# Kernel optimization log

Hardware: AMD Instinct MI355X
Metric: run time of the kernel (lower is better)

## Reference

```python
import jax, jax.numpy as jnp
import numpy as np
import math

D, H, DK, DFF, B, T, K = 512, 8, 64, 2048, 8, 512, 31
P = 2 * T - 1  # rel-pos length


def _ln(x, g, b, eps=1e-5):
    mu = jnp.mean(x, -1, keepdims=True)
    var = jnp.var(x, -1, keepdims=True)
    return (x - mu) * jax.lax.rsqrt(var + eps) * g + b


def _silu(x):
    return x * jax.nn.sigmoid(x)


def _rel_shift(x):
    # x: [B,H,T,P] -> NeMo-style relative shift
    b, h, t, p = x.shape
    x = jnp.pad(x, ((0, 0), (0, 0), (0, 0), (1, 0)))
    x = x.reshape(b, h, p + 1, t)
    return x[:, :, 1:, :].reshape(b, h, t, p)


def _forward(x, pos_emb, ln1_g, ln1_b, ff1_w1, ff1_b1, ff1_w2, ff1_b2,
             lna_g, lna_b, wq, bq, wk, bk, wv, bv, wo, bo, wpos, pbu, pbv,
             lnc_g, lnc_b, pw1_w, pw1_b, dw_w, dw_b, cln_g, cln_b, pw2_w, pw2_b,
             ln2_g, ln2_b, ff2_w1, ff2_b1, ff2_w2, ff2_b2, lno_g, lno_b):
    b, t, d = x.shape
    h, dk = pbu.shape
    # FF1 (half-step residual)
    r = x
    y = _ln(x, ln1_g, ln1_b)
    y = _silu(y @ ff1_w1 + ff1_b1) @ ff1_w2 + ff1_b2
    r = r + 0.5 * y
    # Rel-pos multi-head attention
    y = _ln(r, lna_g, lna_b)
    q = (y @ wq + bq).reshape(b, t, h, dk)
    k = (y @ wk + bk).reshape(b, t, h, dk)
    v = (y @ wv + bv).reshape(b, t, h, dk)
    p = (pos_emb @ wpos).reshape(pos_emb.shape[0], -1, h, dk)[0]  # [P,H,dk]
    ac = jnp.einsum('bthd,bshd->bhts', q + pbu, k)
    bd = jnp.einsum('bthd,phd->bhtp', q + pbv, p)
    bd = _rel_shift(bd)[..., :t]
    attn = jax.nn.softmax((ac + bd) / math.sqrt(dk), axis=-1)
    o = jnp.einsum('bhts,bshd->bthd', attn, v).reshape(b, t, d) @ wo + bo
    r = r + o
    # Conformer convolution module (layer_norm variant)
    y = _ln(r, lnc_g, lnc_b)
    y = y @ pw1_w + pw1_b                       # [B,T,2D] pointwise conv1
    a, g = jnp.split(y, 2, axis=-1)
    y = a * jax.nn.sigmoid(g)                   # GLU over channels
    y = jnp.transpose(y, (0, 2, 1))             # [B,D,T]
    pad = (dw_w.shape[1] - 1) // 2
    y = jax.lax.conv_general_dilated(
        y, dw_w[:, None, :], (1,), [(pad, pad)],
        feature_group_count=d, dimension_numbers=('NCH', 'OIH', 'NCH'))
    y = y + dw_b[None, :, None]
    y = jnp.transpose(y, (0, 2, 1))             # [B,T,D]
    y = _ln(y, cln_g, cln_b)
    y = _silu(y) @ pw2_w + pw2_b                # pointwise conv2
    r = r + y
    # FF2 (half-step residual)
    y = _ln(r, ln2_g, ln2_b)
    y = _silu(y @ ff2_w1 + ff2_b1) @ ff2_w2 + ff2_b2
    r = r + 0.5 * y
    return _ln(r, lno_g, lno_b)


def setup_inputs() -> dict:
    key = jax.random.key(0)
    ks = iter(jax.random.split(key, 64))
    rn = lambda shape, s=0.05: jax.random.normal(next(ks), shape, dtype=jnp.float32) * s
    ones = lambda n: jnp.ones((n,), jnp.float32)
    zeros = lambda n: jnp.zeros((n,), jnp.float32)
    return dict(
        x=jax.random.normal(next(ks), (B, T, D), jnp.float32),
        pos_emb=jax.random.normal(next(ks), (1, P, D), jnp.float32),
        ln1_g=ones(D), ln1_b=zeros(D),
        ff1_w1=rn((D, DFF)), ff1_b1=zeros(DFF), ff1_w2=rn((DFF, D)), ff1_b2=zeros(D),
        lna_g=ones(D), lna_b=zeros(D),
        wq=rn((D, D)), bq=zeros(D), wk=rn((D, D)), bk=zeros(D),
        wv=rn((D, D)), bv=zeros(D), wo=rn((D, D)), bo=zeros(D),
        wpos=rn((D, D)), pbu=rn((H, DK)), pbv=rn((H, DK)),
        lnc_g=ones(D), lnc_b=zeros(D),
        pw1_w=rn((D, 2 * D)), pw1_b=zeros(2 * D),
        dw_w=rn((D, K)), dw_b=zeros(D),
        cln_g=ones(D), cln_b=zeros(D),
        pw2_w=rn((D, D)), pw2_b=zeros(D),
        ln2_g=ones(D), ln2_b=zeros(D),
        ff2_w1=rn((D, DFF)), ff2_b1=zeros(DFF), ff2_w2=rn((DFF, D)), ff2_b2=zeros(D),
        lno_g=ones(D), lno_b=zeros(D))


def reference(x, pos_emb, ln1_g, ln1_b, ff1_w1, ff1_b1, ff1_w2, ff1_b2,
              lna_g, lna_b, wq, bq, wk, bk, wv, bv, wo, bo, wpos, pbu, pbv,
              lnc_g, lnc_b, pw1_w, pw1_b, dw_w, dw_b, cln_g, cln_b, pw2_w, pw2_b,
              ln2_g, ln2_b, ff2_w1, ff2_b1, ff2_w2, ff2_b2, lno_g, lno_b):
    return _forward(x, pos_emb, ln1_g, ln1_b, ff1_w1, ff1_b1, ff1_w2, ff1_b2,
                    lna_g, lna_b, wq, bq, wk, bk, wv, bv, wo, bo, wpos, pbu, pbv,
                    lnc_g, lnc_b, pw1_w, pw1_b, dw_w, dw_b, cln_g, cln_b, pw2_w, pw2_b,
                    ln2_g, ln2_b, ff2_w1, ff2_b1, ff2_w2, ff2_b2, lno_g, lno_b)
```

## Files before the change

### kernel.cpp

```cpp
#include <hip/hip_runtime.h>
#include <hip/hip_bf16.h>

#define Bb 8
#define Tt 512
#define Dd 512
#define Hh 8
#define DKk 64
#define DFFf 2048
#define Pp 1023
#define KCc 31
#define BTt 4096
#define QS 1536

typedef __hip_bfloat16 bf16;
typedef __attribute__((ext_vector_type(8))) short short8;
typedef __attribute__((ext_vector_type(4))) short s4v;
typedef __attribute__((ext_vector_type(4))) float f32x4;

union BFU { __hip_bfloat16 h; short s; };
static __device__ __forceinline__ short bfbits(float f) {
    BFU u; u.h = __float2bfloat16(f); return u.s;
}
static __device__ __forceinline__ float bff(short s) {
    BFU u; u.s = s; return __bfloat162float(u.h);
}
static __device__ __forceinline__ unsigned pk2(float a, float b) {
    return (unsigned)(unsigned short)bfbits(a) | ((unsigned)(unsigned short)bfbits(b) << 16);
}

static __device__ __forceinline__ int dflag(const void* lg) {
    return ((const unsigned*)lg)[0] == 0x3F803F80u;
}

#define GLD16(g, l) __builtin_amdgcn_global_load_lds(                          \
    (const __attribute__((address_space(1))) void*)(g),                        \
    (__attribute__((address_space(3))) void*)(l), 16, 0, 0)

#define XCD_SWZ(bxs, bys)                                                     \
    int nwg_ = gridDim.x * gridDim.y;                                         \
    int w_ = blockIdx.y * gridDim.x + blockIdx.x;                             \
    int sw_ = (w_ & 7) * (nwg_ >> 3) + (w_ >> 3);                             \
    int bxs = sw_ % gridDim.x, bys = sw_ / gridDim.x;

struct CvtDesc { const void* src; unsigned n; unsigned off; unsigned startBlk; };
struct CvtArgs { CvtDesc d[32]; };

__global__ __launch_bounds__(256) void cvt_batch_k(CvtArgs args, int ncv,
                                                   bf16* __restrict__ dst,
                                                   const void* __restrict__ lg) {
    int bid = blockIdx.x;
    int ti = 0;
    while (ti + 1 < ncv && bid >= (int)args.d[ti + 1].startBlk) ti++;
    CvtDesc de = args.d[ti];
    unsigned i = (bid - de.startBlk) * 256u + threadIdx.x;
    if (i >= de.n) return;
    float v;
    if (dflag(lg)) v = __bfloat162float(((const bf16*)de.src)[i]);
    else           v = ((const float*)de.src)[i];
    dst[de.off + i] = __float2bfloat16(v);
}

struct TD { const void* src; unsigned doff, R, C, startBlk; };
struct TArgs { TD d[11]; };

__global__ __launch_bounds__(256) void transpose_batch_k(TArgs ta, bf16* __restrict__ wt,
                                                         const void* __restrict__ lg) {
    int bid = blockIdx.x;
    int ti = 0;
    while (ti + 1 < 11 && bid >= (int)ta.d[ti + 1].startBlk) ti++;
    TD t = ta.d[ti];
    int tile = bid - t.startBlk;
    int ntc = t.C >> 5;
    int tr = tile / ntc, tc = tile % ntc;
    __shared__ short tl[32][33];
    short* out = (short*)wt + t.doff;
    int tx = threadIdx.x & 31, ty = threadIdx.x >> 5;
    int fl = dflag(lg);
#pragma unroll
    for (int i = 0; i < 32; i += 8) {
        size_t idx = (size_t)(tr * 32 + ty + i) * t.C + tc * 32 + tx;
        short v;
        if (fl) v = ((const short*)t.src)[idx];
        else    v = bfbits(((const float*)t.src)[idx]);
        tl[ty + i][tx] = v;
    }
    __syncthreads();
#pragma unroll
    for (int i = 0; i < 32; i += 8)
        out[(size_t)(tc * 32 + ty + i) * t.R + tr * 32 + tx] = tl[tx][ty + i];
}

__global__ __launch_bounds__(256) void prep_misc_k(const void* __restrict__ dww, bf16* __restrict__ dwT,
                                                   const void* __restrict__ bq, const void* __restrict__ bk,
                                                   const void* __restrict__ bv, bf16* __restrict__ bqkv,
                                                   bf16* __restrict__ pF,
                                                   const void* __restrict__ lg) {
    int i = blockIdx.x * 256 + threadIdx.x;
    int fl = dflag(lg);
    if (i < Dd * KCc) {
        int d = i / KCc, j = i % KCc;
        short v = fl ? ((const short*)dww)[i] : bfbits(((const float*)dww)[i]);
        ((short*)dwT)[j * Dd + d] = v;
    } else if (i < Dd * KCc + QS) {
        int j = i - Dd * KCc;
        const void* s = (j < 512) ? bq : ((j < 1024) ? bk : bv);
        int idx = j & 511;
        short v = fl ? ((const short*)s)[idx] : bfbits(((const float*)s)[idx]);
        ((short*)bqkv)[j] = v;
    } else {
        int j2 = i - Dd * KCc - QS;
        if (j2 < 512) {
            int h = j2 >> 6, ksp = (j2 >> 5) & 1, qd = (j2 >> 3) & 3, e = j2 & 7;
            ((short*)pF)[(size_t)h * 65536 + ksp * 512 + qd * 128 + e] = 0;
        }
    }
}

template <int SILU>
__global__ __launch_bounds__(256) void ln_k(const float* __restrict__ in,
                                            const bf16* __restrict__ g,
                                            const bf16* __restrict__ b,
                                            bf16* __restrict__ out) {
    int row = blockIdx.x;
    int tid = threadIdx.x;
    float2 v = ((const float2*)(in + (size_t)row * Dd))[tid];
    float s = v.x + v.y;
    float ss = v.x * v.x + v.y * v.y;
#pragma unroll
    for (int off = 32; off > 0; off >>= 1) {
        s += __shfl_xor(s, off);
        ss += __shfl_xor(ss, off);
    }
    __shared__ float red[2][4];
    int wid = tid >> 6;
    if ((tid & 63) == 0) { red[0][wid] = s; red[1][wid] = ss; }
    __syncthreads();
    float S = red[0][0] + red[0][1] + red[0][2] + red[0][3];
    float SS = red[1][0] + red[1][1] + red[1][2] + red[1][3];
    float mean = S * (1.0f / Dd);
    float var = SS * (1.0f / Dd) - mean * mean;
    float rstd = rsqrtf(var + 1e-5f);
    unsigned gp = *(const unsigned*)((const short*)g + 2 * tid);
    unsigned bp = *(const unsigned*)((const short*)b + 2 * tid);
    float o0 = (v.x - mean) * rstd * bff((short)(gp & 0xFFFF)) + bff((short)(bp & 0xFFFF));
    float o1 = (v.y - mean) * rstd * bff((short)(gp >> 16)) + bff((short)(bp >> 16));
    if (SILU) {
        o0 = o0 / (1.0f + __expf(-o0));
        o1 = o1 / (1.0f + __expf(-o1));
    }
    *(unsigned*)((short*)out + (size_t)row * Dd + 2 * tid) = pk2(o0, o1);
}

__global__ __launch_bounds__(256) void ln_x_k(const void* __restrict__ x,
                                              const bf16* __restrict__ g,
                                              const bf16* __restrict__ b,
                                              float* __restrict__ r,
                                              bf16* __restrict__ out,
                                              const void* __restrict__ lg) {
    int row = blockIdx.x;
    int tid = threadIdx.x;
    size_t base = (size_t)row * Dd;
    float v0, v1;
    if (dflag(lg)) {
        unsigned xp = *(const unsigned*)((const short*)x + base + 2 * tid);
        v0 = bff((short)(xp & 0xFFFF));
        v1 = bff((short)(xp >> 16));
    } else {
        float2 xv = ((const float2*)((const float*)x + base))[tid];
        v0 = xv.x; v1 = xv.y;
    }
    ((float2*)(r + base))[tid] = make_float2(v0, v1);
    float s = v0 + v1;
    float ss = v0 * v0 + v1 * v1;
#pragma unroll
    for (int off = 32; off > 0; off >>= 1) {
        s += __shfl_xor(s, off);
        ss += __shfl_xor(ss, off);
    }
    __shared__ float red[2][4];
    int wid = tid >> 6;
    if ((tid & 63) == 0) { red[0][wid] = s; red[1][wid] = ss; }
    __syncthreads();
    float S = red[0][0] + red[0][1] + red[0][2] + red[0][3];
    float SS = red[1][0] + red[1][1] + red[1][2] + red[1][3];
    float mean = S * (1.0f / Dd);
    float var = SS * (1.0f / Dd) - mean * mean;
    float rstd = rsqrtf(var + 1e-5f);
    unsigned gp = *(const unsigned*)((const short*)g + 2 * tid);
    unsigned bp = *(const unsigned*)((const short*)b + 2 * tid);
    float o0 = (v0 - mean) * rstd * bff((short)(gp & 0xFFFF)) + bff((short)(bp & 0xFFFF));
    float o1 = (v1 - mean) * rstd * bff((short)(gp >> 16)) + bff((short)(bp >> 16));
    *(unsigned*)((short*)out + base + 2 * tid) = pk2(o0, o1);
}

__global__ __launch_bounds__(256) void ln_out_k(const float* __restrict__ in,
                                                const bf16* __restrict__ g,
                                                const bf16* __restrict__ b,
                                                void* __restrict__ out,
                                                const void* __restrict__ lg) {
    int row = blockIdx.x;
    int tid = threadIdx.x;
    size_t base = (size_t)row * Dd;
    float2 v = ((const float2*)(in + base))[tid];
    float s = v.x + v.y;
    float ss = v.x * v.x + v.y * v.y;
#pragma unroll
    for (int off = 32; off > 0; off >>= 1) {
        s += __shfl_xor(s, off);
        ss += __shfl_xor(ss, off);
    }
    __shared__ float red[2][4];
    int wid = tid >> 6;
    if ((tid & 63) == 0) { red[0][wid] = s; red[1][wid] = ss; }
    __syncthreads();
    float S = red[0][0] + red[0][1] + red[0][2] + red[0][3];
    float SS = red[1][0] + red[1][1] + red[1][2] + red[1][3];
    float mean = S * (1.0f / Dd);
    float var = SS * (1.0f / Dd) - mean * mean;
    float rstd = rsqrtf(var + 1e-5f);
    unsigned gp = *(const unsigned*)((const short*)g + 2 * tid);
    unsigned bp = *(const unsigned*)((const short*)b + 2 * tid);
    float o0 = (v.x - mean) * rstd * bff((short)(gp & 0xFFFF)) + bff((short)(bp & 0xFFFF));
    float o1 = (v.y - mean) * rstd * bff((short)(gp >> 16)) + bff((short)(bp >> 16));
    if (dflag(lg)) {
        *(unsigned*)((short*)out + base + 2 * tid) = pk2(o0, o1);
    } else {
        ((float2*)((float*)out + base))[tid] = make_float2(o0, o1);
    }
}

template <int BM, int BN, int BK, int WM, int WN, typename CT, int ACT, int RES, int VT>
__global__ __launch_bounds__(256) void gemm_mfma_k(const bf16* __restrict__ Abf,
                                                   const bf16* __restrict__ WT,
                                                   const bf16* __restrict__ bias,
                                                   const float* __restrict__ resid,
                                                   CT* __restrict__ C,
                                                   bf16* __restrict__ vt,
                                                   bf16* __restrict__ kf,
                                                   bf16* __restrict__ qf,
                                                   int M, int N, int Kd, float alpha) {
    constexpr int MT = WM / 16, NT = WN / 16;
    constexpr int WX = BN / WN;
    constexpr int CPB = BK / 8;
    constexpr int KS = BK / 32;
    __shared__ __align__(16) short As[BM * BK];
    __shared__ __align__(16) short Bs[BN * BK];
    int tid = threadIdx.x;
    int wid = tid >> 6, lane = tid & 63;
    int lm = lane & 15, quad = lane >> 4;
    int wy = wid / WX, wx = wid % WX;
    XCD_SWZ(bxs, bys);
    int bm = bys * BM, bn = bxs * BN;
    const short* Ag = (const short*)Abf;
    const short* Bg = (const short*)WT;

    f32x4 acc[MT][NT] = {};

    for (int k0 = 0; k0 < Kd; k0 += BK) {
#pragma unroll
        for (int it = 0; it < BM * CPB / 256; it++) {
            int c = it * 256 + tid;
            int row = c / CPB;
            int q = (c % CPB) ^ (row & 7);
            int gr = bm + row;
            if (gr > M - 1) gr = M - 1;
            GLD16(Ag + (size_t)gr * Kd + k0 + q * 8, As + (it * 256 + wid * 64) * 8);
        }
#pragma unroll
        for (int it = 0; it < BN * CPB / 256; it++) {
            int c = it * 256 + tid;
            int row = c / CPB;
            int q = (c % CPB) ^ (row & 7);
            GLD16(Bg + (size_t)(bn + row) * Kd + k0 + q * 8, Bs + (it * 256 + wid * 64) * 8);
        }
        __syncthreads();
        short8 af[MT][KS], bfv[NT][KS];
#pragma unroll
        for (int mt = 0; mt < MT; mt++) {
            int row = wy * WM + mt * 16 + lm;
#pragma unroll
            for (int ks = 0; ks < KS; ks++)
                af[mt][ks] = *(const short8*)&As[row * BK + (((ks * 4 + quad) ^ (row & 7)) * 8)];
        }
#pragma unroll
        for (int nt = 0; nt < NT; nt++) {
            int row = wx * WN + nt * 16 + lm;
#pragma unroll
            for (int ks = 0; ks < KS; ks++)
                bfv[nt][ks] = *(const short8*)&Bs[row * BK + (((ks * 4 + quad) ^ (row & 7)) * 8)];
        }
#pragma unroll
        for (int ks = 0; ks < KS; ks++)
#pragma unroll
            for (int mt = 0; mt < MT; mt++)
#pragma unroll
                for (int nt = 0; nt < NT; nt++)
                    acc[mt][nt] = __builtin_amdgcn_mfma_f32_16x16x32_bf16(af[mt][ks], bfv[nt][ks], acc[mt][nt], 0, 0, 0);
        __syncthreads();
    }

#pragma unroll
    for (int mt = 0; mt < MT; mt++) {
#pragma unroll
        for (int nt = 0; nt < NT; nt++) {
            int gcol = bn + wx * WN + nt * 16 + lm;
            int growb = bm + wy * WM + mt * 16 + quad * 4;
            if (VT == 1 && gcol >= 1024) {
                int hd = gcol - 1024;
                int h = hd >> 6, d = hd & 63;
                int b = growb >> 9, tt = growb & 511;
                float bi = __bfloat162float(bias[gcol]);
                s4v pk;
#pragma unroll
                for (int r = 0; r < 4; r++) pk[r] = bfbits(acc[mt][nt][r] + bi);
                size_t base = (((((size_t)b * 8 + h) * 16 + (tt >> 5)) * 4 + (d >> 4)) * 64 +
                               (((tt >> 3) & 3) * 16 + (d & 15))) * 8 + (tt & 7);
                *(s4v*)((short*)vt + base) = pk;
            } else if (VT == 1 && gcol >= 512) {
                int hd = gcol - 512;
                int h = hd >> 6, kk = hd & 63;
                int b = growb >> 9, tt = growb & 511;
                float bi = __bfloat162float(bias[gcol]);
                size_t base2 = ((((size_t)b * 8 + h) * 32 + (tt >> 4)) * 2 + (kk >> 5)) * 512;
                int qd = (kk >> 3) & 3, e = kk & 7;
#pragma unroll
                for (int r = 0; r < 4; r++)
                    ((short*)kf)[base2 + (size_t)(qd * 16 + (tt & 15) + r) * 8 + e] =
                        bfbits(acc[mt][nt][r] + bi);
            } else if (VT == 1) {
                int h = gcol >> 6, kk = gcol & 63;
                int b = growb >> 9, tt = growb & 511;
                float bi = __bfloat162float(bias[gcol]);
                size_t base2 = ((((size_t)b * 8 + h) * 32 + (tt >> 4)) * 2 + (kk >> 5)) * 512;
                int qd = (kk >> 3) & 3, e = kk & 7;
#pragma unroll
                for (int r = 0; r < 4; r++)
                    ((short*)qf)[base2 + (size_t)(qd * 16 + (tt & 15) + r) * 8 + e] =
                        bfbits(acc[mt][nt][r] + bi);
            } else if (VT == 2) {
                int h = gcol >> 6, kk = gcol & 63;
                int ksp = kk >> 5, qd = (kk >> 3) & 3, e = kk & 7;
#pragma unroll
                for (int r = 0; r < 4; r++) {
                    int grow = growb + r;
                    if (grow >= M) continue;
                    int p1 = grow + 1;
                    int J = p1 >> 4, lmz = p1 & 15;
                    ((short*)vt)[(size_t)(h * 64 + J) * 1024 + ksp * 512 + (qd * 16 + lmz) * 8 + e] =
                        bfbits(acc[mt][nt][r]);
                }
            } else {
#pragma unroll
                for (int r = 0; r < 4; r++) {
                    int grow = growb + r;
                    if (grow >= M) continue;
                    float v = acc[mt][nt][r];
                    if (bias) v += __bfloat162float(bias[gcol]);
                    if (ACT == 1) v = v / (1.0f + __expf(-v));
                    if (RES == 1) v = resid[(size_t)grow * N + gcol] + alpha * v;
                    C[(size_t)grow * N + gcol] = (CT)v;
                }
            }
        }
    }
}

__global__ __launch_bounds__(256) void gemm_glu_k(const bf16* __restrict__ Abf,
                                                  const bf16* __restrict__ WT,
                                                  const bf16* __restrict__ bias,
                                                  bf16* __restrict__ C) {
    constexpr int BM = 64, BN = 64, BK = 64, WM = 32, WN = 32;
    constexpr int MT = WM / 16, NT = WN / 16, WX = BN / WN, CPB = BK / 8, KS = BK / 32;
    __shared__ __align__(16) short As[BM * BK];
    __shared__ __align__(16) short Bs[2 * BN * BK];
    int tid = threadIdx.x;
    int wid = tid >> 6, lane = tid & 63;
    int lm = lane & 15, quad = lane >> 4;
    int wy = wid / WX, wx = wid % WX;
    XCD_SWZ(bxs, bys);
    int bm = bys * BM, bn = bxs * BN;
    const short* Ag = (const short*)Abf;
    const short* Bg = (const short*)WT;

    f32x4 acc[MT][NT][2] = {};

    for (int k0 = 0; k0 < Dd; k0 += BK) {
#pragma unroll
        for (int it = 0; it < BM * CPB / 256; it++) {
            int c = it * 256 + tid;
            int row = c / CPB;
            int q = (c % CPB) ^ (row & 7);
            GLD16(Ag + (size_t)(bm + row) * Dd + k0 + q * 8, As + (it * 256 + wid * 64) * 8);
        }
#pragma unroll
        for (int it = 0; it < 2 * BN * CPB / 256; it++) {
            int c = it * 256 + tid;
            int row = c / CPB;
            int q = (c % CPB) ^ (row & 7);
            int wrow = (row < BN) ? (bn + row) : (512 + bn + row - BN);
            GLD16(Bg + (size_t)wrow * Dd + k0 + q * 8, Bs + (it * 256 + wid * 64) * 8);
        }
        __syncthreads();
        short8 af[MT][KS], bfv[NT][2][KS];
#pragma unroll
        for (int mt = 0; mt < MT; mt++) {
            int row = wy * WM + mt * 16 + lm;
#pragma unroll
            for (int ks = 0; ks < KS; ks++)
                af[mt][ks] = *(const short8*)&As[row * BK + (((ks * 4 + quad) ^ (row & 7)) * 8)];
        }
#pragma unroll
        for (int nt = 0; nt < NT; nt++) {
#pragma unroll
            for (int hf = 0; hf < 2; hf++) {
                int row = hf * BN + wx * WN + nt * 16 + lm;
#pragma unroll
                for (int ks = 0; ks < KS; ks++)
                    bfv[nt][hf][ks] = *(const short8*)&Bs[row * BK + (((ks * 4 + quad) ^ (row & 7)) * 8)];
            }
        }
#pragma unroll
        for (int ks = 0; ks < KS; ks++)
#pragma unroll
            for (int mt = 0; mt < MT; mt++)
#pragma unroll
                for (int nt = 0; nt < NT; nt++) {
                    acc[mt][nt][0] = __builtin_amdgcn_mfma_f32_16x16x32_bf16(af[mt][ks], bfv[nt][0][ks], acc[mt][nt][0], 0, 0, 0);
                    acc[mt][nt][1] = __builtin_amdgcn_mfma_f32_16x16x32_bf16(af[mt][ks], bfv[nt][1][ks], acc[mt][nt][1], 0, 0, 0);
                }
        __syncthreads();
    }

#pragma unroll
    for (int mt = 0; mt < MT; mt++) {
#pragma unroll
        for (int nt = 0; nt < NT; nt++) {
#pragma unroll
            for (int r = 0; r < 4; r++) {
                int grow = bm + wy * WM + mt * 16 + quad * 4 + r;
                int gcol = bn + wx * WN + nt * 16 + lm;
                float va = acc[mt][nt][0][r] + __bfloat162float(bias[gcol]);
                float vg = acc[mt][nt][1][r] + __bfloat162float(bias[512 + gcol]);
                float v = va / (1.0f + __expf(-vg));
                C[(size_t)grow * Dd + gcol] = __float2bfloat16(v);
            }
        }
    }
}

#define PST 520
#define OST 72

__global__ __launch_bounds__(256, 4) void attn_mfma_k(const bf16* __restrict__ qF,
                                                      const bf16* __restrict__ kF,
                                                      const bf16* __restrict__ pF,
                                                      const bf16* __restrict__ vF,
                                                      const bf16* __restrict__ pbu,
                                                      const bf16* __restrict__ pbv,
                                                      bf16* __restrict__ out) {
    __shared__ __align__(16) short Pl[16 * PST];
    __shared__ __align__(16) float redm[16][4];
    __shared__ __align__(16) float reds[16][4];
    int tid = threadIdx.x;
    int wid = tid >> 6;
    int lane = tid & 63;
    int lm = lane & 15;
    int quad = lane >> 4;
    int bidx = (blockIdx.x & 7) * 256 + (blockIdx.x >> 3);
    int b = bidx >> 8;
    int h = (bidx >> 5) & 7;
    int t0 = (bidx & 31) * 16;

    short8 qu[2], qv[2];
    {
        const short* qa = (const short*)qF +
            ((size_t)((b * 8 + h) * 32 + (t0 >> 4)) * 2) * 512 + lane * 8;
        const short* pbus = (const short*)pbu + h * DKk + quad * 8;
        const short* pbvs = (const short*)pbv + h * DKk + quad * 8;
#pragma unroll
        for (int ksp = 0; ksp < 2; ksp++) {
            short8 raw = *(const short8*)(qa + ksp * 512);
            short8 bu = *(const short8*)(pbus + ksp * 32);
            short8 bv = *(const short8*)(pbvs + ksp * 32);
#pragma unroll
            for (int j = 0; j < 8; j++) {
                float qf2 = bff(raw[j]);
                qu[ksp][j] = bfbits(qf2 + bff(bu[j]));
                qv[ksp][j] = bfbits(qf2 + bff(bv[j]));
            }
        }
    }

    const float scale = 0.125f;
    const short* kFs = (const short*)kF + ((size_t)(b * 8 + h) * 32) * 1024;
    const short* pFs = (const short*)pF + ((size_t)h * 64) * 1024;
    int Jbase = 32 - (t0 >> 4) + wid * 8;

    f32x4 dprev = {0.f, 0.f, 0.f, 0.f};
    {
        const short* pa = pFs + (size_t)(Jbase - 1) * 1024 + lane * 8;
        dprev = __builtin_amdgcn_mfma_f32_16x16x32_bf16(qv[0], *(const short8*)pa, dprev, 0, 0, 0);
        dprev = __builtin_amdgcn_mfma_f32_16x16x32_bf16(qv[1], *(const short8*)(pa + 512), dprev, 0, 0, 0);
    }

    f32x4 sreg[8];
#pragma unroll
    for (int i = 0; i < 8; i++) {
        int st = wid * 8 + i;
        f32x4 ac = {0.f, 0.f, 0.f, 0.f};
        f32x4 dcur = {0.f, 0.f, 0.f, 0.f};
        const short* ka = kFs + (size_t)st * 1024 + lane * 8;
        const short* pa = pFs + (size_t)(Jbase + i) * 1024 + lane * 8;
        ac = __builtin_amdgcn_mfma_f32_16x16x32_bf16(qu[0], *(const short8*)ka, ac, 0, 0, 0);
        ac = __builtin_amdgcn_mfma_f32_16x16x32_bf16(qu[1], *(const short8*)(ka + 512), ac, 0, 0, 0);
        dcur = __builtin_amdgcn_mfma_f32_16x16x32_bf16(qv[0], *(const short8*)pa, dcur, 0, 0, 0);
        dcur = __builtin_amdgcn_mfma_f32_16x16x32_bf16(qv[1], *(const short8*)(pa + 512), dcur, 0, 0, 0);
#pragma unroll
        for (int r = 0; r < 4; r++) {
            int m = quad * 4 + r;
            int j = (lm - m) & 15;
            int srcl = quad * 16 + j;
            float b2 = __shfl(dcur[r], srcl, 64);
            float b1 = __shfl(dprev[r], srcl, 64);
            float bd = (lm >= m) ? b2 : b1;
            sreg[i][r] = scale * (ac[r] + bd);
        }
        dprev = dcur;
    }

    float mrow[4];
#pragma unroll
    for (int r = 0; r < 4; r++) {
        float m = sreg[0][r];
#pragma unroll
        for (int i = 1; i < 8; i++) m = fmaxf(m, sreg[i][r]);
#pragma unroll
        for (int off = 1; off < 16; off <<= 1) m = fmaxf(m, __shfl_xor(m, off));
        mrow[r] = m;
    }
    if (lm < 4) {
        float v = (lm == 0) ? mrow[0] : (lm == 1) ? mrow[1] : (lm == 2) ? mrow[2] : mrow[3];
        redm[quad * 4 + lm][wid] = v;
    }
    __syncthreads();

    float gm[4], srow[4];
#pragma unroll
    for (int r = 0; r < 4; r++) {
        float4 mv = *(const float4*)&redm[quad * 4 + r][0];
        gm[r] = fmaxf(fmaxf(mv.x, mv.y), fmaxf(mv.z, mv.w));
        srow[r] = 0.f;
    }
#pragma unroll
    for (int i = 0; i < 8; i++) {
        int col = (wid * 8 + i) * 16 + lm;
#pragma unroll
        for (int r = 0; r < 4; r++) {
            float e = __expf(sreg[i][r] - gm[r]);
            srow[r] += e;
            Pl[(quad * 4 + r) * PST + col] = bfbits(e);
        }
    }
#pragma unroll
    for (int r = 0; r < 4; r++) {
#pragma unroll
        for (int off = 1; off < 16; off <<= 1) srow[r] += __shfl_xor(srow[r], off);
    }
    if (lm < 4) {
        float v = (lm == 0) ? srow[0] : (lm == 1) ? srow[1] : (lm == 2) ? srow[2] : srow[3];
        reds[quad * 4 + lm][wid] = v;
    }
    __syncthreads();

    float lsum[4];
#pragma unroll
    for (int r = 0; r < 4; r++) {
        float4 sv = *(const float4*)&reds[quad * 4 + r][0];
        lsum[r] = (sv.x + sv.y) + (sv.z + sv.w);
    }

    int d0 = wid * 16;
    const short* va = (const short*)vF + (size_t)(b * 8 + h) * 32768 + wid * 512 + lane * 8;
    const short* parow = Pl + (size_t)lm * PST;
    f32x4 o0 = {0.f, 0.f, 0.f, 0.f};
    f32x4 o1 = {0.f, 0.f, 0.f, 0.f};
#pragma unroll
    for (int ksp = 0; ksp < 16; ksp += 2) {
        short8 a0 = *(const short8*)(parow + ksp * 32 + quad * 8);
        short8 v0 = *(const short8*)(va + (size_t)ksp * 2048);
        short8 a1 = *(const short8*)(parow + (ksp + 1) * 32 + quad * 8);
        short8 v1 = *(const short8*)(va + (size_t)(ksp + 1) * 2048);
        o0 = __builtin_amdgcn_mfma_f32_16x16x32_bf16(a0, v0, o0, 0, 0, 0);
        o1 = __builtin_amdgcn_mfma_f32_16x16x32_bf16(a1, v1, o1, 0, 0, 0);
    }
    f32x4 o = o0 + o1;

    __syncthreads();
#pragma unroll
    for (int r = 0; r < 4; r++)
        Pl[(quad * 4 + r) * OST + d0 + lm] = bfbits(o[r] / lsum[r]);
    __syncthreads();
    {
        int row = tid >> 4, c4 = (tid & 15) * 4;
        s4v ov = *(const s4v*)&Pl[row * OST + c4];
        *(s4v*)((short*)out + (size_t)(b * Tt + t0 + row) * Dd + h * DKk + c4) = ov;
    }
}

__global__ __launch_bounds__(256) void dwconv_ln_k(const bf16* __restrict__ in,
                                                   const bf16* __restrict__ wT,
                                                   const bf16* __restrict__ bdw,
                                                   const bf16* __restrict__ g,
                                                   const bf16* __restrict__ bb,
                                                   bf16* __restrict__ out) {
    int row = blockIdx.x * 4 + (threadIdx.x >> 6);
    int lane = threadIdx.x & 63;
    int d0 = lane * 8;
    int t = row & 511, b = row >> 9;
    const short* ins = (const short*)in + (size_t)b * Tt * Dd;
    const short* wts = (const short*)wT;
    float acc[8];
    short8 bv = *(const short8*)((const short*)bdw + d0);
#pragma unroll
    for (int e = 0; e < 8; e++) acc[e] = bff(bv[e]);
#pragma unroll
    for (int j = 0; j < KCc; j++) {
        int tt = t + j - 15;
        if (tt < 0 || tt >= Tt) continue;
        short8 iv = *(const short8*)(ins + (size_t)tt * Dd + d0);
        short8 wv = *(const short8*)(wts + j * Dd + d0);
#pragma unroll
        for (int e = 0; e < 8; e++) acc[e] += bff(iv[e]) * bff(wv[e]);
    }
    float s = 0.f, ss = 0.f;
#pragma unroll
    for (int e = 0; e < 8; e++) { s += acc[e]; ss += acc[e] * acc[e]; }
#pragma unroll
    for (int off = 32; off > 0; off >>= 1) {
        s += __shfl_xor(s, off);
        ss += __shfl_xor(ss, off);
    }
    float mean = s * (1.0f / Dd);
    float var = ss * (1.0f / Dd) - mean * mean;
    float rstd = rsqrtf(var + 1e-5f);
    short8 gv = *(const short8*)((const short*)g + d0);
    short8 bbv = *(const short8*)((const short*)bb + d0);
    short8 ov;
#pragma unroll
    for (int e = 0; e < 8; e++) {
        float o = (acc[e] - mean) * rstd * bff(gv[e]) + bff(bbv[e]);
        o = o / (1.0f + __expf(-o));
        ov[e] = bfbits(o);
    }
    *(short8*)((short*)out + (size_t)row * Dd + d0) = ov;
}

extern "C" void kernel_launch(void* const* d_in, const int* in_sizes, int n_in,
                              void* d_out, int out_size, void* d_ws, size_t ws_size,
                              hipStream_t stream) {
    char* base = (char*)d_ws;
    bf16* wb = (bf16*)(base + 256);

    size_t woff[39];
    size_t acc = 0;
    for (int i = 1; i < 39; i++) { woff[i] = acc; acc += (size_t)in_sizes[i]; }
    size_t wbytes = (2 * acc + 255) & ~(size_t)255;

    const size_t NBT = (size_t)BTt * Dd;
    float* r   = (float*)((char*)wb + wbytes);
    bf16* a    = (bf16*)((char*)r + NBT * 4);
    bf16* big  = a + NBT;
    bf16* pbuf = big + (size_t)BTt * DFFf;
    bf16* wt   = pbuf + (size_t)Pp * Dd;

    const void* lg = d_in[2];

    bf16* c_pos   = wb + woff[1];
    bf16* c_ln1g  = wb + woff[2],  *c_ln1b = wb + woff[3];
    bf16* c_f1b1  = wb + woff[5];
    bf16* c_f1b2  = wb + woff[7];
    bf16* c_lnag  = wb + woff[8],  *c_lnab = wb + woff[9];
    bf16* c_bo    = wb + woff[17];
    bf16* c_pbu   = wb + woff[19], *c_pbv  = wb + woff[20];
    bf16* c_lncg  = wb + woff[21], *c_lncb = wb + woff[22];
    bf16* c_p1b   = wb + woff[24];
    bf16* c_dwb   = wb + woff[26];
    bf16* c_clng  = wb + woff[27], *c_clnb = wb + woff[28];
    bf16* c_p2b   = wb + woff[30];
    bf16* c_ln2g  = wb + woff[31], *c_ln2b = wb + woff[32];
    bf16* c_f2b1  = wb + woff[34];
    bf16* c_f2b2  = wb + woff[36];
    bf16* c_lnog  = wb + woff[37], *c_lnob = wb + woff[38];

    const int tin[11]  = {4, 6, 10, 12, 14, 16, 18, 23, 29, 33, 35};
    const unsigned tR[11] = {512, 2048, 512, 512, 512, 512, 512, 512, 512, 512, 2048};
    const unsigned tC[11] = {2048, 512, 512, 512, 512, 512, 512, 1024, 512, 2048, 512};
    size_t toff[11]; size_t tacc = 0;
    for (int i = 0; i < 11; i++) { toff[i] = tacc; tacc += (size_t)tR[i] * tC[i]; }
    bf16* t_f1w1 = wt + toff[0];
    bf16* t_f1w2 = wt + toff[1];
    bf16* t_wqkv = wt + toff[2];
    bf16* t_wo   = wt + toff[5];
    bf16* t_wpos = wt + toff[6];
    bf16* t_p1w  = wt + toff[7];
    bf16* t_p2w  = wt + toff[8];
    bf16* t_f2w1 = wt + toff[9];
    bf16* t_f2w2 = wt + toff[10];
    bf16* bias_qkv = wt + tacc;
    bf16* dwT      = bias_qkv + QS;
    bf16* vTb      = dwT + KCc * Dd;
    bf16* kFb      = vTb + (size_t)2097152;
    bf16* pFb      = kFb + (size_t)2097152;
    bf16* qFb      = pFb + (size_t)524288;

    dim3 blk(256);

    bool skip[39] = {};
    for (int i = 0; i < 11; i++) skip[tin[i]] = true;
    skip[11] = skip[13] = skip[15] = skip[25] = true;
    CvtArgs ca;
    int ncv = 0;
    unsigned blkacc = 0;
    for (int i = 1; i < 39; i++) {
        if (skip[i]) continue;
        ca.d[ncv].src = d_in[i];
        ca.d[ncv].n = (unsigned)in_sizes[i];
        ca.d[ncv].off = (unsigned)woff[i];
        ca.d[ncv].startBlk = blkacc;
        blkacc += (unsigned)((in_sizes[i] + 255) / 256);
        ncv++;
    }
    cvt_batch_k<<<blkacc, blk, 0, stream>>>(ca, ncv, wb, lg);

    TArgs ta;
    unsigned tblk = 0;
    for (int i = 0; i < 11; i++) {
        ta.d[i].src = d_in[tin[i]];
        ta.d[i].doff = (unsigned)toff[i];
        ta.d[i].R = tR[i];
        ta.d[i].C = tC[i];
        ta.d[i].startBlk = tblk;
        tblk += (tR[i] >> 5) * (tC[i] >> 5);
    }
    transpose_batch_k<<<tblk, blk, 0, stream>>>(ta, wt, lg);
    prep_misc_k<<<(Dd * KCc + QS + 512 + 255) / 256, blk, 0, stream>>>(
        d_in[25], dwT, d_in[11], d_in[13], d_in[15], bias_qkv, pFb, lg);

    auto g128 = [](int M, int N) { return dim3(N / 128, M / 128); };
    auto g64  = [](int M, int N) { return dim3(N / 64, (M + 63) / 64); };

    ln_x_k<<<BTt, blk, 0, stream>>>(d_in[0], c_ln1g, c_ln1b, r, a, lg);
    gemm_mfma_k<128, 128, 128, 64, 64, bf16, 1, 0, 0><<<g128(BTt, DFFf), blk, 0, stream>>>(
        a, t_f1w1, c_f1b1, nullptr, big, nullptr, nullptr, nullptr, BTt, DFFf, Dd, 0.f);
    gemm_mfma_k<64, 64, 128, 32, 32, float, 0, 1, 0><<<g64(BTt, Dd), blk, 0, stream>>>(
        big, t_f1w2, c_f1b2, r, r, nullptr, nullptr, nullptr, BTt, Dd, DFFf, 0.5f);

    bf16* cb = big + 3 * NBT;
    ln_k<0><<<BTt, blk, 0, stream>>>(r, c_lnag, c_lnab, a);
    gemm_mfma_k<128, 64, 64, 64, 32, bf16, 0, 0, 1><<<dim3(QS / 64, BTt / 128), blk, 0, stream>>>(
        a, t_wqkv, bias_qkv, nullptr, (bf16*)nullptr, vTb, kFb, qFb, BTt, QS, Dd, 0.f);
    gemm_mfma_k<64, 64, 64, 32, 32, bf16, 0, 0, 2><<<g64(Pp, Dd), blk, 0, stream>>>(
        c_pos, t_wpos, nullptr, nullptr, (bf16*)nullptr, pFb, nullptr, nullptr, Pp, Dd, Dd, 0.f);
    attn_mfma_k<<<Bb * Hh * (Tt / 16), blk, 0, stream>>>(qFb, kFb, pFb, vTb, c_pbu, c_pbv, cb);
    gemm_mfma_k<64, 64, 64, 32, 32, float, 0, 1, 0><<<g64(BTt, Dd), blk, 0, stream>>>(
        cb, t_wo, c_bo, r, r, nullptr, nullptr, nullptr, BTt, Dd, Dd, 1.0f);

    bf16* gluo = big + 2 * NBT;
    ln_k<0><<<BTt, blk, 0, stream>>>(r, c_lncg, c_lncb, a);
    gemm_glu_k<<<dim3(Dd / 64, BTt / 64), blk, 0, stream>>>(a, t_p1w, c_p1b, gluo);
    dwconv_ln_k<<<BTt / 4, blk, 0, stream>>>(gluo, dwT, c_dwb, c_clng, c_clnb, a);
    gemm_mfma_k<64, 64, 64, 32, 32, float, 0, 1, 0><<<g64(BTt, Dd), blk, 0, stream>>>(
        a, t_p2w, c_p2b, r, r, nullptr, nullptr, nullptr, BTt, Dd, Dd, 1.0f);

    ln_k<0><<<BTt, blk, 0, stream>>>(r, c_ln2g, c_ln2b, a);
    gemm_mfma_k<128, 128, 128, 64, 64, bf16, 1, 0, 0><<<g128(BTt, DFFf), blk, 0, stream>>>(
        a, t_f2w1, c_f2b1, nullptr, big, nullptr, nullptr, nullptr, BTt, DFFf, Dd, 0.f);
    gemm_mfma_k<64, 64, 128, 32, 32, float, 0, 1, 0><<<g64(BTt, Dd), blk, 0, stream>>>(
        big, t_f2w2, c_f2b2, r, r, nullptr, nullptr, nullptr, BTt, Dd, DFFf, 0.5f);

    ln_out_k<<<BTt, blk, 0, stream>>>(r, c_lnog, c_lnob, d_out, lg);
}
```

Measured before the change: 390.6 us.

## Split-K the FF down-projection GEMMs with a separate reduction kernel

The two FF second GEMMs (K=2048) now run with a z-dimension of 2. Each z-slice covers half of K and writes fp32 partials to a scratch buffer, and a new row-wise kernel sums the partials, adds the bias and applies the half-step residual. The aim is to double the block count for these long-K GEMMs (512 to 1024 blocks) so the GPU is better filled. In exchange it adds an extra launch and about 16MB of fp32 partial traffic per GEMM, and it assumes the scratch region after qFb is allocated.

```diff
diff --git a/kernel.cpp b/kernel.cpp
--- a/kernel.cpp
+++ b/kernel.cpp
@@ -229,6 +229,21 @@
     }
 }
 
+__global__ __launch_bounds__(256) void red_k(const float* __restrict__ part,
+                                             const bf16* __restrict__ bias,
+                                             float* __restrict__ r, float alpha) {
+    int row = blockIdx.x;
+    int tid = threadIdx.x;
+    size_t base = (size_t)row * Dd;
+    float2 a0 = ((const float2*)(part + base))[tid];
+    float2 a1 = ((const float2*)(part + (size_t)BTt * Dd + base))[tid];
+    float2 rv = ((const float2*)(r + base))[tid];
+    unsigned bp = *(const unsigned*)((const short*)bias + 2 * tid);
+    rv.x += alpha * (a0.x + a1.x + bff((short)(bp & 0xFFFF)));
+    rv.y += alpha * (a0.y + a1.y + bff((short)(bp >> 16)));
+    ((float2*)(r + base))[tid] = rv;
+}
+
 template <int BM, int BN, int BK, int WM, int WN, typename CT, int ACT, int RES, int VT>
 __global__ __launch_bounds__(256) void gemm_mfma_k(const bf16* __restrict__ Abf,
                                                    const bf16* __restrict__ WT,
@@ -238,7 +253,7 @@
                                                    bf16* __restrict__ vt,
                                                    bf16* __restrict__ kf,
                                                    bf16* __restrict__ qf,
-                                                   int M, int N, int Kd, float alpha) {
+                                                   int M, int N, int Kd, int lda, float alpha) {
     constexpr int MT = WM / 16, NT = WN / 16;
     constexpr int WX = BN / WN;
     constexpr int CPB = BK / 8;
@@ -251,8 +266,9 @@
     int wy = wid / WX, wx = wid % WX;
     XCD_SWZ(bxs, bys);
     int bm = bys * BM, bn = bxs * BN;
-    const short* Ag = (const short*)Abf;
-    const short* Bg = (const short*)WT;
+    int koff = blockIdx.z * Kd;
+    const short* Ag = (const short*)Abf + koff;
+    const short* Bg = (const short*)WT + koff;
 
     f32x4 acc[MT][NT] = {};
 
@@ -264,14 +280,14 @@
             int q = (c % CPB) ^ (row & 7);
             int gr = bm + row;
             if (gr > M - 1) gr = M - 1;
-            GLD16(Ag + (size_t)gr * Kd + k0 + q * 8, As + (it * 256 + wid * 64) * 8);
+            GLD16(Ag + (size_t)gr * lda + k0 + q * 8, As + (it * 256 + wid * 64) * 8);
         }
 #pragma unroll
         for (int it = 0; it < BN * CPB / 256; it++) {
             int c = it * 256 + tid;
             int row = c / CPB;
             int q = (c % CPB) ^ (row & 7);
-            GLD16(Bg + (size_t)(bn + row) * Kd + k0 + q * 8, Bs + (it * 256 + wid * 64) * 8);
+            GLD16(Bg + (size_t)(bn + row) * lda + k0 + q * 8, Bs + (it * 256 + wid * 64) * 8);
         }
         __syncthreads();
         short8 af[MT][KS], bfv[NT][KS];
@@ -348,6 +364,13 @@
                     int J = p1 >> 4, lmz = p1 & 15;
                     ((short*)vt)[(size_t)(h * 64 + J) * 1024 + ksp * 512 + (qd * 16 + lmz) * 8 + e] =
                         bfbits(acc[mt][nt][r]);
+                }
+            } else if (RES == 2) {
+                size_t zoff = (size_t)blockIdx.z * M * N;
+#pragma unroll
+                for (int r = 0; r < 4; r++) {
+                    int grow = growb + r;
+                    C[zoff + (size_t)grow * N + gcol] = (CT)acc[mt][nt][r];
                 }
             } else {
 #pragma unroll
@@ -712,6 +735,7 @@
     bf16* kFb      = vTb + (size_t)2097152;
     bf16* pFb      = kFb + (size_t)2097152;
     bf16* qFb      = pFb + (size_t)524288;
+    float* part    = (float*)(qFb + (size_t)2097152);
 
     dim3 blk(256);
 
@@ -751,32 +775,34 @@
 
     ln_x_k<<<BTt, blk, 0, stream>>>(d_in[0], c_ln1g, c_ln1b, r, a, lg);
     gemm_mfma_k<128, 128, 128, 64, 64, bf16, 1, 0, 0><<<g128(BTt, DFFf), blk, 0, stream>>>(
-        a, t_f1w1, c_f1b1, nullptr, big, nullptr, nullptr, nullptr, BTt, DFFf, Dd, 0.f);
-    gemm_mfma_k<64, 64, 128, 32, 32, float, 0, 1, 0><<<g64(BTt, Dd), blk, 0, stream>>>(
-        big, t_f1w2, c_f1b2, r, r, nullptr, nullptr, nullptr, BTt, Dd, DFFf, 0.5f);
+        a, t_f1w1, c_f1b1, nullptr, big, nullptr, nullptr, nullptr, BTt, DFFf, Dd, Dd, 0.f);
+    gemm_mfma_k<64, 64, 128, 32, 32, float, 0, 2, 0><<<dim3(Dd / 64, BTt / 64, 2), blk, 0, stream>>>(
+        big, t_f1w2, nullptr, nullptr, part, nullptr, nullptr, nullptr, BTt, Dd, DFFf / 2, DFFf, 0.f);
+    red_k<<<BTt, blk, 0, stream>>>(part, c_f1b2, r, 0.5f);
 
     bf16* cb = big + 3 * NBT;
     ln_k<0><<<BTt, blk, 0, stream>>>(r, c_lnag, c_lnab, a);
     gemm_mfma_k<128, 64, 64, 64, 32, bf16, 0, 0, 1><<<dim3(QS / 64, BTt / 128), blk, 0, stream>>>(
-        a, t_wqkv, bias_qkv, nullptr, (bf16*)nullptr, vTb, kFb, qFb, BTt, QS, Dd, 0.f);
+        a, t_wqkv, bias_qkv, nullptr, (bf16*)nullptr, vTb, kFb, qFb, BTt, QS, Dd, Dd, 0.f);
     gemm_mfma_k<64, 64, 64, 32, 32, bf16, 0, 0, 2><<<g64(Pp, Dd), blk, 0, stream>>>(
-        c_pos, t_wpos, nullptr, nullptr, (bf16*)nullptr, pFb, nullptr, nullptr, Pp, Dd, Dd, 0.f);
+        c_pos, t_wpos, nullptr, nullptr, (bf16*)nullptr, pFb, nullptr, nullptr, Pp, Dd, Dd, Dd, 0.f);
     attn_mfma_k<<<Bb * Hh * (Tt / 16), blk, 0, stream>>>(qFb, kFb, pFb, vTb, c_pbu, c_pbv, cb);
     gemm_mfma_k<64, 64, 64, 32, 32, float, 0, 1, 0><<<g64(BTt, Dd), blk, 0, stream>>>(
-        cb, t_wo, c_bo, r, r, nullptr, nullptr, nullptr, BTt, Dd, Dd, 1.0f);
+        cb, t_wo, c_bo, r, r, nullptr, nullptr, nullptr, BTt, Dd, Dd, Dd, 1.0f);
 
     bf16* gluo = big + 2 * NBT;
     ln_k<0><<<BTt, blk, 0, stream>>>(r, c_lncg, c_lncb, a);
     gemm_glu_k<<<dim3(Dd / 64, BTt / 64), blk, 0, stream>>>(a, t_p1w, c_p1b, gluo);
     dwconv_ln_k<<<BTt / 4, blk, 0, stream>>>(gluo, dwT, c_dwb, c_clng, c_clnb, a);
     gemm_mfma_k<64, 64, 64, 32, 32, float, 0, 1, 0><<<g64(BTt, Dd), blk, 0, stream>>>(
-        a, t_p2w, c_p2b, r, r, nullptr, nullptr, nullptr, BTt, Dd, Dd, 1.0f);
+        a, t_p2w, c_p2b, r, r, nullptr, nullptr, nullptr, BTt, Dd, Dd, Dd, 1.0f);
 
     ln_k<0><<<BTt, blk, 0, stream>>>(r, c_ln2g, c_ln2b, a);
     gemm_mfma_k<128, 128, 128, 64, 64, bf16, 1, 0, 0><<<g128(BTt, DFFf), blk, 0, stream>>>(
-        a, t_f2w1, c_f2b1, nullptr, big, nullptr, nullptr, nullptr, BTt, DFFf, Dd, 0.f);
-    gemm_mfma_k<64, 64, 128, 32, 32, float, 0, 1, 0><<<g64(BTt, Dd), blk, 0, stream>>>(
-        big, t_f2w2, c_f2b2, r, r, nullptr, nullptr, nullptr, BTt, Dd, DFFf, 0.5f);
+        a, t_f2w1, c_f2b1, nullptr, big, nullptr, nullptr, nullptr, BTt, DFFf, Dd, Dd, 0.f);
+    gemm_mfma_k<64, 64, 128, 32, 32, float, 0, 2, 0><<<dim3(Dd / 64, BTt / 64, 2), blk, 0, stream>>>(
+        big, t_f2w2, nullptr, nullptr, part, nullptr, nullptr, nullptr, BTt, Dd, DFFf / 2, DFFf, 0.f);
+    red_k<<<BTt, blk, 0, stream>>>(part, c_f2b2, r, 0.5f);
 
     ln_out_k<<<BTt, blk, 0, stream>>>(r, c_lnog, c_lnob, d_out, lg);
 }
```

Result: no change. 387.8 us (-0.7%).
